# Kernel optimization log

Measured on AMD Instinct MI355X. Metric: run time of the kernel, lower is better.

Reference implementation:

```python
import jax, jax.numpy as jnp
import numpy as np


def _lstm_scan(x_proj, Wh, b, c0, h0):
    """Run an LSTM over time. x_proj: [S, B, 4F] (inputs pre-projected by Wi).
    Flax OptimizedLSTMCell gate order: i, f, g, o."""
    def step(carry, xp):
        c, h = carry
        z = xp + h @ Wh + b                      # [B, 4F]
        i, f, g, o = jnp.split(z, 4, axis=-1)
        c = jax.nn.sigmoid(f) * c + jax.nn.sigmoid(i) * jnp.tanh(g)
        h = jax.nn.sigmoid(o) * jnp.tanh(c)
        return (c, h), h
    return jax.lax.scan(step, (c0, h0), x_proj)


def setup_inputs() -> dict:
    key = jax.random.key(0)
    ks = jax.random.split(key, 7)
    B, S, H, F = 16, 4096, 256, 256
    sH = 1.0 / np.sqrt(H)
    sF = 1.0 / np.sqrt(F)
    return {
        "inputs": jax.random.normal(ks[0], (B, S, H), jnp.float32),
        "Wi_fw": jax.random.normal(ks[1], (H, 4 * F), jnp.float32) * sH,
        "Wh_fw": jax.random.normal(ks[2], (F, 4 * F), jnp.float32) * sF,
        "b_fw": jnp.zeros((4 * F,), jnp.float32),
        "Wi_rv": jax.random.normal(ks[3], (H, 4 * F), jnp.float32) * sH,
        "Wh_rv": jax.random.normal(ks[4], (F, 4 * F), jnp.float32) * sF,
        "b_rv": jnp.zeros((4 * F,), jnp.float32),
    }


def reference(inputs, Wi_fw, Wh_fw, b_fw, Wi_rv, Wh_rv, b_rv):
    B, S, H = inputs.shape
    F = Wh_fw.shape[0]
    x = inputs.transpose(1, 0, 2)                       # [S, B, H] time-major
    zeros = jnp.zeros((B, F), inputs.dtype)

    # forward direction: pre-project all timesteps (one big GEMM), then scan
    xp_fw = jnp.einsum('sbh,hf->sbf', x, Wi_fw)         # [S, B, 4F]
    (c_fw, h_fw), hs_fw = _lstm_scan(xp_fw, Wh_fw, b_fw, zeros, zeros)

    # reverse direction: flax Bidirectional flips time, runs, flips back
    xp_rv = jnp.einsum('sbh,hf->sbf', x[::-1], Wi_rv)   # [S, B, 4F]
    (c_rv, h_rv), hs_rv = _lstm_scan(xp_rv, Wh_rv, b_rv, zeros, zeros)
    hs_rv = hs_rv[::-1]

    # merge_fn = _concatenate: [forward, reverse] along features
    output = jnp.concatenate([hs_fw, hs_rv], axis=-1).transpose(1, 0, 2)  # [B, S, 2F]
    return output, (c_fw, h_fw), (c_rv, h_rv)
```

## Files before the change

kernel.cpp:

```cpp
#include <hip/hip_runtime.h>

#define S_LEN 4096
#define BATCH 16
#define HID   256
#define GATE4 1024

typedef __bf16 bf16x8 __attribute__((ext_vector_type(8)));
typedef float  f32x4  __attribute__((ext_vector_type(4)));

union FragU {
    unsigned short u[8];
    bf16x8 v;
    uint4  q;
};

__device__ __forceinline__ unsigned short f2bf(float f) {
    unsigned u = __builtin_bit_cast(unsigned, f);
    u += 0x7fffu + ((u >> 16) & 1u);
    return (unsigned short)(u >> 16);
}
__device__ __forceinline__ float bf2f(unsigned short s) {
    unsigned u = ((unsigned)s) << 16;
    return __builtin_bit_cast(float, u);
}
__device__ __forceinline__ float sigmoid_f(float x) {
    return 1.f / (1.f + __expf(-x));
}
__device__ __forceinline__ float tanh_f(float x) {
    float e = __expf(2.f * x);
    return 1.f - 2.f / (e + 1.f);
}

__global__ void init_ctrl(unsigned int* c) {
    if (threadIdx.x < 128) c[threadIdx.x] = (threadIdx.x == 16) ? 0xFFFFFFFFu : 0u;
}

__global__ __launch_bounds__(256, 2) void xp_gemm(
    const float* __restrict__ X,
    const float* __restrict__ Wi_fw, const float* __restrict__ b_fw,
    const float* __restrict__ Wi_rv, const float* __restrict__ b_rv,
    unsigned short* __restrict__ xp_fw, unsigned short* __restrict__ xp_rv)
{
    const int dir = blockIdx.z;
    const float* Wi   = dir ? Wi_rv : Wi_fw;
    const float* bias = dir ? b_rv  : b_fw;
    unsigned short* xp = dir ? xp_rv : xp_fw;

    __shared__ unsigned short As[64][40];
    __shared__ unsigned short Bs[64][40];

    const int tid  = threadIdx.x;
    const int lane = tid & 63;
    const int wid  = tid >> 6;
    const int quad = lane >> 4;
    const int l16  = lane & 15;
    const int wm = wid >> 1, wn = wid & 1;

    const int r0 = blockIdx.x * 64;
    const int n0 = blockIdx.y * 64;

    const int ai = tid & 63;
    const int ak = (tid >> 6) * 8;
    const int bk = tid >> 3;
    const int bj = (tid & 7) * 8;

    const int r  = r0 + ai;
    const int t  = r >> 4, bb = r & 15;
    const int t_eff = dir ? (S_LEN - 1 - t) : t;
    const float* Arow = X + ((size_t)bb * S_LEN + t_eff) * HID;

    f32x4 acc[2][2];
    #pragma unroll
    for (int i = 0; i < 2; ++i)
        #pragma unroll
        for (int j = 0; j < 2; ++j) { acc[i][j][0]=0.f; acc[i][j][1]=0.f; acc[i][j][2]=0.f; acc[i][j][3]=0.f; }

    for (int kb = 0; kb < HID / 32; ++kb) {
        {
            const float* p = Arow + kb * 32 + ak;
            float4 v0 = *(const float4*)p;
            float4 v1 = *(const float4*)(p + 4);
            FragU fu;
            fu.u[0]=f2bf(v0.x); fu.u[1]=f2bf(v0.y); fu.u[2]=f2bf(v0.z); fu.u[3]=f2bf(v0.w);
            fu.u[4]=f2bf(v1.x); fu.u[5]=f2bf(v1.y); fu.u[6]=f2bf(v1.z); fu.u[7]=f2bf(v1.w);
            *(uint4*)&As[ai][ak] = fu.q;
        }
        {
            const float* p = Wi + (size_t)(kb * 32 + bk) * GATE4 + n0 + bj;
            float4 v0 = *(const float4*)p;
            float4 v1 = *(const float4*)(p + 4);
            unsigned short tmp[8] = { f2bf(v0.x), f2bf(v0.y), f2bf(v0.z), f2bf(v0.w),
                                      f2bf(v1.x), f2bf(v1.y), f2bf(v1.z), f2bf(v1.w) };
            #pragma unroll
            for (int jj = 0; jj < 8; ++jj) Bs[bj + jj][bk] = tmp[jj];
        }
        __syncthreads();

        bf16x8 a0 = *(const bf16x8*)&As[wm * 32 + l16][quad * 8];
        bf16x8 a1 = *(const bf16x8*)&As[wm * 32 + 16 + l16][quad * 8];
        bf16x8 B0 = *(const bf16x8*)&Bs[wn * 32 + l16][quad * 8];
        bf16x8 B1 = *(const bf16x8*)&Bs[wn * 32 + 16 + l16][quad * 8];
        acc[0][0] = __builtin_amdgcn_mfma_f32_16x16x32_bf16(a0, B0, acc[0][0], 0, 0, 0);
        acc[0][1] = __builtin_amdgcn_mfma_f32_16x16x32_bf16(a0, B1, acc[0][1], 0, 0, 0);
        acc[1][0] = __builtin_amdgcn_mfma_f32_16x16x32_bf16(a1, B0, acc[1][0], 0, 0, 0);
        acc[1][1] = __builtin_amdgcn_mfma_f32_16x16x32_bf16(a1, B1, acc[1][1], 0, 0, 0);
        __syncthreads();
    }

    #pragma unroll
    for (int am = 0; am < 2; ++am)
        #pragma unroll
        for (int bn = 0; bn < 2; ++bn) {
            int ncol = n0 + wn * 32 + bn * 16 + l16;
            float bv = bias[ncol];
            #pragma unroll
            for (int rr = 0; rr < 4; ++rr) {
                int rrow = r0 + wm * 32 + am * 16 + quad * 4 + rr;
                float v = acc[am][bn][rr] + bv;
                xp[(size_t)rrow * GATE4 + ncol] = f2bf(v);
            }
        }
}

__global__ __launch_bounds__(512, 2) void lstm_rec(
    const float* __restrict__ Wh_fw, const float* __restrict__ Wh_rv,
    const unsigned short* __restrict__ xp_fw, const unsigned short* __restrict__ xp_rv,
    float* __restrict__ out,
    float* __restrict__ finals,
    unsigned short* __restrict__ exch,
    unsigned int* __restrict__ ctrl)
{
    const int tid  = threadIdx.x;
    __shared__ int role_s;

    if (tid == 0) {
        unsigned xcc;
        asm volatile("s_getreg_b32 %0, hwreg(HW_REG_XCC_ID)" : "=s"(xcc));
        xcc &= 7u;
        int role = -1;
        unsigned idx = atomicAdd(&ctrl[8u + xcc], 1u);
        if (idx < 4u) {
            if (idx == 3u) atomicCAS(&ctrl[16], 0xFFFFFFFFu, xcc);
            unsigned w;
            while ((w = __hip_atomic_fetch_add(&ctrl[16], 0u, __ATOMIC_RELAXED,
                                               __HIP_MEMORY_SCOPE_AGENT)) == 0xFFFFFFFFu)
                __builtin_amdgcn_s_sleep(2);
            if (w == xcc) role = (int)idx;
        }
        role_s = role;
    }
    __syncthreads();
    const int role = role_s;
    if (role < 0) return;

    const int dir  = role >> 1;
    const int half = role & 1;
    const float* Wh = dir ? Wh_rv : Wh_fw;
    const unsigned short* xp = dir ? xp_rv : xp_fw;

    const int lane = tid & 63;
    const int wid  = tid >> 6;
    const int quad = lane >> 4;
    const int l16  = lane & 15;

    const int fbase = half * 128 + wid * 16;
    const int floc  = wid * 16 + l16;
    const int po    = (1 - half) * 128;

    __shared__ unsigned short hbuf[16][264];

    for (int i = tid; i < 16 * 264; i += 512) ((unsigned short*)hbuf)[i] = 0;

    bf16x8 Bfrag[4][8];
    #pragma unroll
    for (int g = 0; g < 4; ++g) {
        int col = g * 256 + fbase + l16;
        #pragma unroll
        for (int kt = 0; kt < 8; ++kt) {
            FragU fu;
            #pragma unroll
            for (int j = 0; j < 8; ++j) {
                int k = kt * 32 + quad * 8 + j;
                fu.u[j] = f2bf(Wh[(size_t)k * GATE4 + col]);
            }
            Bfrag[g][kt] = fu.v;
        }
    }

    float cst[4]  = {0.f, 0.f, 0.f, 0.f};
    float hval[4] = {0.f, 0.f, 0.f, 0.f};

    unsigned int* myseq = ctrl + (dir * 2 + half) * 32;
    unsigned int* pseq  = ctrl + (dir * 2 + (1 - half)) * 32;

    const size_t lanebase = (size_t)(quad * 4) * GATE4 + fbase + l16;

    unsigned short xpA[4][4], xpB[4][4];
    {
        const unsigned short* x0 = xp + lanebase;
        const unsigned short* x1 = xp + (size_t)BATCH * GATE4 + lanebase;
        #pragma unroll
        for (int g = 0; g < 4; ++g)
            #pragma unroll
            for (int rr = 0; rr < 4; ++rr) {
                xpA[g][rr] = x0[(size_t)rr * GATE4 + g * 256];
                xpB[g][rr] = x1[(size_t)rr * GATE4 + g * 256];
            }
    }

    const int prc = tid & 127;
    const int pg4 = tid >> 7;

    __syncthreads();

    auto step = [&](int s, unsigned short (&xpc)[4][4]) {
        const int parity = s & 1;
        const bool last = (s == S_LEN - 1);

        bf16x8 Afrag[8];
        #pragma unroll
        for (int kt = 0; kt < 8; ++kt)
            Afrag[kt] = *(const bf16x8*)&hbuf[l16][kt * 32 + quad * 8];

        asm volatile("s_waitcnt lgkmcnt(0)" ::: "memory");
        __builtin_amdgcn_s_barrier();

        f32x4 accg[4];
        #pragma unroll
        for (int g = 0; g < 4; ++g) { accg[g][0]=0.f; accg[g][1]=0.f; accg[g][2]=0.f; accg[g][3]=0.f; }
        #pragma unroll
        for (int kt = 0; kt < 8; ++kt) {
            accg[0] = __builtin_amdgcn_mfma_f32_16x16x32_bf16(Afrag[kt], Bfrag[0][kt], accg[0], 0, 0, 0);
            accg[1] = __builtin_amdgcn_mfma_f32_16x16x32_bf16(Afrag[kt], Bfrag[1][kt], accg[1], 0, 0, 0);
            accg[2] = __builtin_amdgcn_mfma_f32_16x16x32_bf16(Afrag[kt], Bfrag[2][kt], accg[2], 0, 0, 0);
            accg[3] = __builtin_amdgcn_mfma_f32_16x16x32_bf16(Afrag[kt], Bfrag[3][kt], accg[3], 0, 0, 0);
        }

        unsigned short hb[4];
        #pragma unroll
        for (int rr = 0; rr < 4; ++rr) {
            float zi = accg[0][rr] + bf2f(xpc[0][rr]);
            float zf = accg[1][rr] + bf2f(xpc[1][rr]);
            float zg = accg[2][rr] + bf2f(xpc[2][rr]);
            float zo = accg[3][rr] + bf2f(xpc[3][rr]);
            float ig = sigmoid_f(zi);
            float fg = sigmoid_f(zf);
            float gg = tanh_f(zg);
            float og = sigmoid_f(zo);
            float c  = fg * cst[rr] + ig * gg;
            cst[rr]  = c;
            float h  = og * tanh_f(c);
            hval[rr] = h;
            hb[rr]   = f2bf(h);
        }

        #pragma unroll
        for (int rr = 0; rr < 4; ++rr)
            hbuf[quad * 4 + rr][fbase + l16] = hb[rr];

        if (!last) {
            unsigned long long pk =
                  (unsigned long long)hb[0]
                | ((unsigned long long)hb[1] << 16)
                | ((unsigned long long)hb[2] << 32)
                | ((unsigned long long)hb[3] << 48);
            unsigned long long* ex = (unsigned long long*)(exch
                + (size_t)(((dir * 2 + parity) * 2) + half) * 2048)
                + ((size_t)floc * 16 + quad * 4) / 4;
            __hip_atomic_store(ex, pk, __ATOMIC_RELAXED, __HIP_MEMORY_SCOPE_AGENT);
            asm volatile("s_waitcnt vmcnt(0)" ::: "memory");
            __builtin_amdgcn_s_barrier();
            if (tid == 0)
                __hip_atomic_store(myseq, (unsigned)(s + 1), __ATOMIC_RELAXED,
                                   __HIP_MEMORY_SCOPE_AGENT);

            while (__hip_atomic_load(pseq, __ATOMIC_RELAXED, __HIP_MEMORY_SCOPE_AGENT)
                   < (unsigned)(s + 1)) { }
            asm volatile("" ::: "memory");

            const unsigned long long* pd = (const unsigned long long*)(exch
                + (size_t)(((dir * 2 + parity) * 2) + (1 - half)) * 2048)
                + ((size_t)prc * 16 + pg4 * 4) / 4;
            unsigned long long v = __hip_atomic_load(pd, __ATOMIC_RELAXED,
                                                     __HIP_MEMORY_SCOPE_AGENT);
            hbuf[pg4 * 4 + 0][po + prc] = (unsigned short)(v);
            hbuf[pg4 * 4 + 1][po + prc] = (unsigned short)(v >> 16);
            hbuf[pg4 * 4 + 2][po + prc] = (unsigned short)(v >> 32);
            hbuf[pg4 * 4 + 3][po + prc] = (unsigned short)(v >> 48);
            asm volatile("s_waitcnt lgkmcnt(0)" ::: "memory");
            __builtin_amdgcn_s_barrier();
        }

        {
            int t_orig = dir ? (S_LEN - 1 - s) : s;
            float* ob = out + (size_t)t_orig * 512 + dir * 256 + fbase + l16;
            #pragma unroll
            for (int rr = 0; rr < 4; ++rr)
                ob[(size_t)(quad * 4 + rr) * S_LEN * 512] = hval[rr];
        }
        if (s + 2 < S_LEN) {
            const unsigned short* xr = xp + (size_t)(s + 2) * (BATCH * GATE4) + lanebase;
            #pragma unroll
            for (int g = 0; g < 4; ++g)
                #pragma unroll
                for (int rr = 0; rr < 4; ++rr)
                    xpc[g][rr] = xr[(size_t)rr * GATE4 + g * 256];
        }
    };

    for (int s2 = 0; s2 < S_LEN; s2 += 2) {
        step(s2,     xpA);
        step(s2 + 1, xpB);
    }

    {
        float* cdst = finals + (dir ? 8192 : 0);
        float* hdst = cdst + 4096;
        #pragma unroll
        for (int rr = 0; rr < 4; ++rr) {
            int m = quad * 4 + rr;
            int f = fbase + l16;
            cdst[m * 256 + f] = cst[rr];
            hdst[m * 256 + f] = hval[rr];
        }
    }
}

extern "C" void kernel_launch(void* const* d_in, const int* in_sizes, int n_in,
                              void* d_out, int out_size, void* d_ws, size_t ws_size,
                              hipStream_t stream)
{
    const float* X     = (const float*)d_in[0];
    const float* Wi_fw = (const float*)d_in[1];
    const float* Wh_fw = (const float*)d_in[2];
    const float* b_fw  = (const float*)d_in[3];
    const float* Wi_rv = (const float*)d_in[4];
    const float* Wh_rv = (const float*)d_in[5];
    const float* b_rv  = (const float*)d_in[6];

    float* out    = (float*)d_out;
    float* finals = out + (size_t)BATCH * S_LEN * 512;

    char* ws = (char*)d_ws;
    unsigned short* xp_fw = (unsigned short*)ws;
    unsigned short* xp_rv = (unsigned short*)(ws + 134217728ull);
    unsigned short* exch  = (unsigned short*)(ws + 268435456ull);
    unsigned int*   ctrl  = (unsigned int*)(ws + 268435456ull + 32768ull);

    init_ctrl<<<1, 128, 0, stream>>>(ctrl);

    dim3 g(65536 / 64, 1024 / 64, 2);
    xp_gemm<<<g, 256, 0, stream>>>(X, Wi_fw, b_fw, Wi_rv, b_rv, xp_fw, xp_rv);

    lstm_rec<<<64, 512, 0, stream>>>(Wh_fw, Wh_rv, xp_fw, xp_rv, out, finals, exch, ctrl);
}
```

Baseline: 13.32 ms.

## Replace sequence-counter handshake with tagged per-thread exchange words and double-buffered hbuf

The cross-block h exchange used to pack data, wait on stores, run a block barrier, publish a sequence counter, then spin on the partner's counter. Now each thread writes 64-bit words that carry the step number alongside the bf16 h values, and the partner polls its own matching words directly until the tag matches. hbuf is double-buffered by step parity, so one barrier per step replaces three. This removes the store-drain wait and the extra barriers from the serial critical path, at the cost of twice as many exchange stores and per-thread spinning on global memory.

```diff
diff --git a/kernel.cpp b/kernel.cpp
--- a/kernel.cpp
+++ b/kernel.cpp
@@ -31,8 +31,10 @@
     return 1.f - 2.f / (e + 1.f);
 }
 
-__global__ void init_ctrl(unsigned int* c) {
-    if (threadIdx.x < 128) c[threadIdx.x] = (threadIdx.x == 16) ? 0xFFFFFFFFu : 0u;
+__global__ void init_ctrl(unsigned int* ctrl, unsigned int* exch4) {
+    int t = threadIdx.x;
+    if (t < 128) ctrl[t] = (t == 16) ? 0xFFFFFFFFu : 0u;
+    for (int i = t; i < 16384; i += 1024) exch4[i] = 0u;
 }
 
 __global__ __launch_bounds__(256, 2) void xp_gemm(
@@ -127,7 +129,7 @@
     const unsigned short* __restrict__ xp_fw, const unsigned short* __restrict__ xp_rv,
     float* __restrict__ out,
     float* __restrict__ finals,
-    unsigned short* __restrict__ exch,
+    char* __restrict__ exch,
     unsigned int* __restrict__ ctrl)
 {
     const int tid  = threadIdx.x;
@@ -167,9 +169,9 @@
     const int floc  = wid * 16 + l16;
     const int po    = (1 - half) * 128;
 
-    __shared__ unsigned short hbuf[16][264];
-
-    for (int i = tid; i < 16 * 264; i += 512) ((unsigned short*)hbuf)[i] = 0;
+    __shared__ unsigned short hbuf[2][16][264];
+
+    for (int i = tid; i < 2 * 16 * 264; i += 512) (&hbuf[0][0][0])[i] = 0;
 
     bf16x8 Bfrag[4][8];
     #pragma unroll
@@ -190,10 +192,16 @@
     float cst[4]  = {0.f, 0.f, 0.f, 0.f};
     float hval[4] = {0.f, 0.f, 0.f, 0.f};
 
-    unsigned int* myseq = ctrl + (dir * 2 + half) * 32;
-    unsigned int* pseq  = ctrl + (dir * 2 + (1 - half)) * 32;
-
     const size_t lanebase = (size_t)(quad * 4) * GATE4 + fbase + l16;
+
+    unsigned long long* exA = (unsigned long long*)(exch
+        + (size_t)(((dir * 2 + 0) * 2) + half) * 8192) + (size_t)tid * 2;
+    unsigned long long* exB = (unsigned long long*)(exch
+        + (size_t)(((dir * 2 + 1) * 2) + half) * 8192) + (size_t)tid * 2;
+    const unsigned long long* pdA = (const unsigned long long*)(exch
+        + (size_t)(((dir * 2 + 0) * 2) + (1 - half)) * 8192) + (size_t)tid * 2;
+    const unsigned long long* pdB = (const unsigned long long*)(exch
+        + (size_t)(((dir * 2 + 1) * 2) + (1 - half)) * 8192) + (size_t)tid * 2;
 
     unsigned short xpA[4][4], xpB[4][4];
     {
@@ -208,22 +216,17 @@
             }
     }
 
-    const int prc = tid & 127;
-    const int pg4 = tid >> 7;
-
     __syncthreads();
 
-    auto step = [&](int s, unsigned short (&xpc)[4][4]) {
-        const int parity = s & 1;
+    auto step = [&](int s, unsigned short (&xpc)[4][4],
+                    unsigned long long* exm, const unsigned long long* pdm) {
+        const int p = s & 1;
         const bool last = (s == S_LEN - 1);
 
         bf16x8 Afrag[8];
         #pragma unroll
         for (int kt = 0; kt < 8; ++kt)
-            Afrag[kt] = *(const bf16x8*)&hbuf[l16][kt * 32 + quad * 8];
-
-        asm volatile("s_waitcnt lgkmcnt(0)" ::: "memory");
-        __builtin_amdgcn_s_barrier();
+            Afrag[kt] = *(const bf16x8*)&hbuf[p][l16][kt * 32 + quad * 8];
 
         f32x4 accg[4];
         #pragma unroll
@@ -254,41 +257,30 @@
             hb[rr]   = f2bf(h);
         }
 
+        if (!last) {
+            const unsigned long long tag = (unsigned long long)(unsigned)(s + 1) << 32;
+            unsigned long long w0 = tag | (unsigned)hb[0] | ((unsigned)hb[1] << 16);
+            unsigned long long w1 = tag | (unsigned)hb[2] | ((unsigned)hb[3] << 16);
+            __hip_atomic_store(exm,     w0, __ATOMIC_RELAXED, __HIP_MEMORY_SCOPE_AGENT);
+            __hip_atomic_store(exm + 1, w1, __ATOMIC_RELAXED, __HIP_MEMORY_SCOPE_AGENT);
+        }
+
         #pragma unroll
         for (int rr = 0; rr < 4; ++rr)
-            hbuf[quad * 4 + rr][fbase + l16] = hb[rr];
+            hbuf[p ^ 1][quad * 4 + rr][fbase + l16] = hb[rr];
 
         if (!last) {
-            unsigned long long pk =
-                  (unsigned long long)hb[0]
-                | ((unsigned long long)hb[1] << 16)
-                | ((unsigned long long)hb[2] << 32)
-                | ((unsigned long long)hb[3] << 48);
-            unsigned long long* ex = (unsigned long long*)(exch
-                + (size_t)(((dir * 2 + parity) * 2) + half) * 2048)
-                + ((size_t)floc * 16 + quad * 4) / 4;
-            __hip_atomic_store(ex, pk, __ATOMIC_RELAXED, __HIP_MEMORY_SCOPE_AGENT);
-            asm volatile("s_waitcnt vmcnt(0)" ::: "memory");
-            __builtin_amdgcn_s_barrier();
-            if (tid == 0)
-                __hip_atomic_store(myseq, (unsigned)(s + 1), __ATOMIC_RELAXED,
-                                   __HIP_MEMORY_SCOPE_AGENT);
-
-            while (__hip_atomic_load(pseq, __ATOMIC_RELAXED, __HIP_MEMORY_SCOPE_AGENT)
-                   < (unsigned)(s + 1)) { }
-            asm volatile("" ::: "memory");
-
-            const unsigned long long* pd = (const unsigned long long*)(exch
-                + (size_t)(((dir * 2 + parity) * 2) + (1 - half)) * 2048)
-                + ((size_t)prc * 16 + pg4 * 4) / 4;
-            unsigned long long v = __hip_atomic_load(pd, __ATOMIC_RELAXED,
-                                                     __HIP_MEMORY_SCOPE_AGENT);
-            hbuf[pg4 * 4 + 0][po + prc] = (unsigned short)(v);
-            hbuf[pg4 * 4 + 1][po + prc] = (unsigned short)(v >> 16);
-            hbuf[pg4 * 4 + 2][po + prc] = (unsigned short)(v >> 32);
-            hbuf[pg4 * 4 + 3][po + prc] = (unsigned short)(v >> 48);
-            asm volatile("s_waitcnt lgkmcnt(0)" ::: "memory");
-            __builtin_amdgcn_s_barrier();
+            const unsigned tag = (unsigned)(s + 1);
+            unsigned long long w0, w1;
+            do {
+                w0 = __hip_atomic_load(pdm,     __ATOMIC_RELAXED, __HIP_MEMORY_SCOPE_AGENT);
+                w1 = __hip_atomic_load(pdm + 1, __ATOMIC_RELAXED, __HIP_MEMORY_SCOPE_AGENT);
+            } while ((unsigned)(w0 >> 32) != tag || (unsigned)(w1 >> 32) != tag);
+
+            hbuf[p ^ 1][quad * 4 + 0][po + floc] = (unsigned short)(w0);
+            hbuf[p ^ 1][quad * 4 + 1][po + floc] = (unsigned short)(w0 >> 16);
+            hbuf[p ^ 1][quad * 4 + 2][po + floc] = (unsigned short)(w1);
+            hbuf[p ^ 1][quad * 4 + 3][po + floc] = (unsigned short)(w1 >> 16);
         }
 
         {
@@ -306,11 +298,16 @@
                 for (int rr = 0; rr < 4; ++rr)
                     xpc[g][rr] = xr[(size_t)rr * GATE4 + g * 256];
         }
+
+        if (!last) {
+            asm volatile("s_waitcnt lgkmcnt(0)" ::: "memory");
+            __builtin_amdgcn_s_barrier();
+        }
     };
 
     for (int s2 = 0; s2 < S_LEN; s2 += 2) {
-        step(s2,     xpA);
-        step(s2 + 1, xpB);
+        step(s2,     xpA, exA, pdA);
+        step(s2 + 1, xpB, exB, pdB);
     }
 
     {
@@ -344,10 +341,10 @@
     char* ws = (char*)d_ws;
     unsigned short* xp_fw = (unsigned short*)ws;
     unsigned short* xp_rv = (unsigned short*)(ws + 134217728ull);
-    unsigned short* exch  = (unsigned short*)(ws + 268435456ull);
-    unsigned int*   ctrl  = (unsigned int*)(ws + 268435456ull + 32768ull);
-
-    init_ctrl<<<1, 128, 0, stream>>>(ctrl);
+    char*           exch  = ws + 268435456ull;
+    unsigned int*   ctrl  = (unsigned int*)(ws + 268435456ull + 65536ull);
+
+    init_ctrl<<<1, 1024, 0, stream>>>(ctrl, (unsigned int*)exch);
 
     dim3 g(65536 / 64, 1024 / 64, 2);
     xp_gemm<<<g, 256, 0, stream>>>(X, Wi_fw, b_fw, Wi_rv, b_rv, xp_fw, xp_rv);
```

Result: faster. 12.02 ms (-9.8%).
